# Optimization experiments

Hardware: AMD Instinct MI355X
Metric: run time of the kernel (lower is better)

## Reference

```python
import jax, jax.numpy as jnp
import numpy as np
import math

D_MODEL = 1024
NUM_HEADS = 16
MAX_LEN = 2048
D_HEAD = D_MODEL // NUM_HEADS
BATCH = 2
SEQ = 2048


def setup_inputs() -> dict:
    root = jax.random.key(0)
    ks = jax.random.split(root, 10)
    s = 1.0 / math.sqrt(D_MODEL)
    return {
        "query": jax.random.normal(ks[0], (BATCH, SEQ, D_MODEL), jnp.float32),
        "key": jax.random.normal(ks[1], (BATCH, SEQ, D_MODEL), jnp.float32),
        "value": jax.random.normal(ks[2], (BATCH, SEQ, D_MODEL), jnp.float32),
        "Wq": jax.random.normal(ks[3], (D_MODEL, D_MODEL), jnp.float32) * s,
        "bq": jax.random.normal(ks[4], (D_MODEL,), jnp.float32) * s,
        "Wk": jax.random.normal(ks[5], (D_MODEL, D_MODEL), jnp.float32) * s,
        "bk": jax.random.normal(ks[6], (D_MODEL,), jnp.float32) * s,
        "Wv": jax.random.normal(ks[7], (D_MODEL, D_MODEL), jnp.float32) * s,
        "bv": jax.random.normal(ks[8], (D_MODEL,), jnp.float32) * s,
        "Er": jax.random.normal(ks[9], (MAX_LEN, D_HEAD), jnp.float32),
    }


def _skew(QEr):
    # QEr: [B, H, S, S] -> pad one zero column on the left, reshape, drop first row
    B, H, R, C = QEr.shape
    padded = jnp.pad(QEr, ((0, 0), (0, 0), (0, 0), (1, 0)))  # [B,H,R,C+1]
    reshaped = padded.reshape(B, H, C + 1, R)
    return reshaped[:, :, 1:, :]  # [B,H,R,C] == Srel


def reference(query, key, value, Wq, bq, Wk, bk, Wv, bv, Er):
    B, S, D = query.shape
    H, dh = NUM_HEADS, D_HEAD
    # nn.Linear: x @ W.T + b
    q = (jnp.einsum("bsd,ed->bse", query, Wq) + bq).reshape(B, S, H, dh).transpose(0, 2, 1, 3)  # [B,H,S,dh]
    k = (jnp.einsum("bsd,ed->bse", key, Wk) + bk).reshape(B, S, H, dh).transpose(0, 2, 1, 3)
    v = (jnp.einsum("bsd,ed->bse", value, Wv) + bv).reshape(B, S, H, dh).transpose(0, 2, 1, 3)
    start = MAX_LEN - S
    Er_s = Er[start:, :]  # [S, dh]
    QEr = jnp.einsum("bhsd,ld->bhsl", q, Er_s)  # [B,H,S,S]
    Srel = _skew(QEr)
    QK = jnp.einsum("bhsd,bhtd->bhst", q, k)
    attn = (QK + Srel) / math.sqrt(dh)
    causal = jnp.tril(jnp.ones((S, S), dtype=bool))
    attn = jnp.where(causal[None, None], attn, -jnp.inf)
    attn = jax.nn.softmax(attn, axis=-1)
    out = jnp.einsum("bhst,bhtd->bhsd", attn, v)  # [B,H,S,dh]
    out = out.transpose(0, 2, 1, 3).reshape(B, S, D)
    return out  # dropout is identity in eval mode
```

## Files before the change

kernel.cpp:

```cpp
#include <hip/hip_runtime.h>
#include <hip/hip_bf16.h>

typedef __attribute__((ext_vector_type(8))) short bf16x8;
typedef __attribute__((ext_vector_type(4))) float f32x4;

#define DEVI __device__ __forceinline__

constexpr int SEQ_   = 2048;
constexpr int HEADS  = 16;
constexpr int DHEAD  = 64;
constexpr int DMODEL = 1024;

DEVI unsigned short f2bf(float x) {
  __hip_bfloat16 h = __float2bfloat16(x);
  return __builtin_bit_cast(unsigned short, h);
}

DEVI f32x4 MFMA(bf16x8 a, bf16x8 b, f32x4 c) {
  return __builtin_amdgcn_mfma_f32_16x16x32_bf16(a, b, c, 0, 0, 0);
}

__global__ void conv3_kernel(const float* s0, const float* s1, const float* s2,
                             unsigned short* d0, unsigned short* d1, unsigned short* d2,
                             int n) {
  const float* s = (blockIdx.y == 0) ? s0 : (blockIdx.y == 1) ? s1 : s2;
  unsigned short* d = (blockIdx.y == 0) ? d0 : (blockIdx.y == 1) ? d1 : d2;
  int i = (blockIdx.x * 256 + threadIdx.x) * 8;
  if (i >= n) return;
  const float4* p = (const float4*)(s + i);
  float4 v0 = p[0], v1 = p[1];
  union { unsigned short u[8]; bf16x8 v; } t;
  t.u[0] = f2bf(v0.x); t.u[1] = f2bf(v0.y); t.u[2] = f2bf(v0.z); t.u[3] = f2bf(v0.w);
  t.u[4] = f2bf(v1.x); t.u[5] = f2bf(v1.y); t.u[6] = f2bf(v1.z); t.u[7] = f2bf(v1.w);
  *(bf16x8*)(d + i) = t.v;
}

__global__ __launch_bounds__(256) void proj3_kernel(
    const unsigned short* __restrict__ X0, const unsigned short* __restrict__ X1,
    const unsigned short* __restrict__ X2,
    const unsigned short* __restrict__ W0, const unsigned short* __restrict__ W1,
    const unsigned short* __restrict__ W2,
    const float* __restrict__ bi0, const float* __restrict__ bi1,
    const float* __restrict__ bi2,
    unsigned short* __restrict__ o0, unsigned short* __restrict__ o1,
    unsigned short* __restrict__ o2) {
  const int z = blockIdx.z;
  const unsigned short* X = (z == 0) ? X0 : (z == 1) ? X1 : X2;
  const unsigned short* W = (z == 0) ? W0 : (z == 1) ? W1 : W2;
  const float* bias        = (z == 0) ? bi0 : (z == 1) ? bi1 : bi2;
  unsigned short* out      = (z == 0) ? o0 : (z == 1) ? o1 : o2;

  __shared__ unsigned short Abuf[2][128 * 32];
  __shared__ unsigned short Bbuf[2][128 * 32];
  const int tid  = threadIdx.x;
  const int lane = tid & 63, wv = tid >> 6;
  const int q = lane >> 4, r = lane & 15;
  const int wrow = wv >> 1, wcol = wv & 1;
  const int rowA0 = blockIdx.x * 128, colB0 = blockIdx.y * 128;

  const char* Ag = (const char*)(X + (size_t)rowA0 * DMODEL);
  const char* Bg = (const char*)(W + (size_t)colB0 * DMODEL);

  f32x4 acc[4][4] = {};

  auto stage = [&](int ks, int buf) {
    const int koff = ks * 64;
#pragma unroll
    for (int i = 0; i < 2; ++i) {
      const int b   = (i * 256 + tid) * 16;
      const int row = b >> 6, col = b & 63;
      __builtin_amdgcn_global_load_lds(
          (const __attribute__((address_space(1))) void*)(Ag + (size_t)row * (DMODEL * 2) + koff + col),
          (__attribute__((address_space(3))) void*)((char*)&Abuf[buf][0] + i * 4096 + wv * 1024),
          16, 0, 0);
      __builtin_amdgcn_global_load_lds(
          (const __attribute__((address_space(1))) void*)(Bg + (size_t)row * (DMODEL * 2) + koff + col),
          (__attribute__((address_space(3))) void*)((char*)&Bbuf[buf][0] + i * 4096 + wv * 1024),
          16, 0, 0);
    }
  };

  stage(0, 0);
  for (int ks = 0; ks < 32; ++ks) {
    __syncthreads();
    if (ks + 1 < 32) stage(ks + 1, (ks + 1) & 1);
    const unsigned short* A  = &Abuf[ks & 1][0];
    const unsigned short* Bt = &Bbuf[ks & 1][0];
    bf16x8 af[4], bfr[4];
#pragma unroll
    for (int t = 0; t < 4; ++t) {
      af[t]  = *(const bf16x8*)(A  + (wrow * 64 + t * 16 + r) * 32 + q * 8);
      bfr[t] = *(const bf16x8*)(Bt + (wcol * 64 + t * 16 + r) * 32 + q * 8);
    }
#pragma unroll
    for (int m = 0; m < 4; ++m)
#pragma unroll
      for (int n = 0; n < 4; ++n)
        acc[m][n] = MFMA(af[m], bfr[n], acc[m][n]);
  }

#pragma unroll
  for (int m = 0; m < 4; ++m) {
#pragma unroll
    for (int n = 0; n < 4; ++n) {
      const int e  = colB0 + wcol * 64 + n * 16 + r;
      const float bv = bias[e];
      const int h = e >> 6, dd = e & 63;
      const int nrow0 = rowA0 + wrow * 64 + m * 16 + q * 4;
      const int bb = nrow0 >> 11, ss0 = nrow0 & 2047;
      const size_t bh = (size_t)(bb * HEADS + h);
      if (z == 0) {
#pragma unroll
        for (int j = 0; j < 4; ++j)
          out[(bh * SEQ_ + (ss0 + j)) * DHEAD + dd] = f2bf(acc[m][n][j] + bv);
      } else if (z == 1) {
        const int kc = dd >> 5, d32 = dd & 31;
#pragma unroll
        for (int j = 0; j < 4; ++j) {
          const int s = ss0 + j;
          out[(((bh * 64 + (s >> 5)) * 2 + kc) * 32 + (s & 31)) * 32 + d32] =
              f2bf(acc[m][n][j] + bv);
        }
      } else {
        const int stile = ss0 >> 5, st = ss0 & 31;
        union { unsigned short u[4]; uint2 v; } pk;
#pragma unroll
        for (int j = 0; j < 4; ++j) pk.u[j] = f2bf(acc[m][n][j] + bv);
        *(uint2*)&out[((bh * 64 + stile) * 64 + dd) * 32 + st] = pk.v;
      }
    }
  }
}

__global__ __launch_bounds__(128, 2) void attn_kernel(const unsigned short* __restrict__ qb,
                                                      const unsigned short* __restrict__ kt,
                                                      const unsigned short* __restrict__ vt,
                                                      const unsigned short* __restrict__ Er,
                                                      float* __restrict__ out) {
  __shared__ unsigned short k_lds[2][2048];
  __shared__ unsigned short v_lds[2][2048];
  __shared__ unsigned short p_lds[2][16][40];

  const int tid  = threadIdx.x;
  const int lane = tid & 63, wv = tid >> 6;
  const int q = lane >> 4, r = lane & 15;

  const int lid = blockIdx.x;
  const int xcd = lid & 7, idx = lid >> 3;
  const int bh  = (xcd << 2) | (idx & 3);
  const int pairidx = idx >> 2;
  const int bb = bh >> 4, hh = bh & 15;

  const unsigned short* qbh = qb + (size_t)bh * SEQ_ * DHEAD;
  const char* ktb = (const char*)(kt + (size_t)bh * 64 * 2048);
  const char* vtb = (const char*)(vt + (size_t)bh * 64 * 2048);

  const f32x4 zero4 = {0.f, 0.f, 0.f, 0.f};

  auto stage = [&](int tile, int buf) {
#pragma unroll
    for (int c = 0; c < 2; ++c) {
      __builtin_amdgcn_global_load_lds(
          (const __attribute__((address_space(1))) void*)(ktb + (size_t)tile * 4096 + (c * 128 + tid) * 16),
          (__attribute__((address_space(3))) void*)((char*)&k_lds[buf][0] + c * 2048 + wv * 1024),
          16, 0, 0);
      __builtin_amdgcn_global_load_lds(
          (const __attribute__((address_space(1))) void*)(vtb + (size_t)tile * 4096 + (c * 128 + tid) * 16),
          (__attribute__((address_space(3))) void*)((char*)&v_lds[buf][0] + c * 2048 + wv * 1024),
          16, 0, 0);
    }
  };

#pragma unroll 1
  for (int si = 0; si < 2; ++si) {
    const int t = si ? pairidx : 63 - pairidx;
    const int nIter = t + 1;
    const int s0 = t * 32 + wv * 16;

    __syncthreads();
    stage(0, 0);

    bf16x8 qf0 = *(const bf16x8*)(qbh + (size_t)(s0 + r) * DHEAD + q * 8);
    bf16x8 qf1 = *(const bf16x8*)(qbh + (size_t)(s0 + r) * DHEAD + 32 + q * 8);

    f32x4 oacc[4] = {};
    float lpart[4] = {0.f, 0.f, 0.f, 0.f};
    f32x4 qer0;
    {
      const int l0 = 2032 - s0 + r;
      bf16x8 e00 = *(const bf16x8*)(Er + (size_t)l0 * DHEAD + q * 8);
      bf16x8 e01 = *(const bf16x8*)(Er + (size_t)l0 * DHEAD + 32 + q * 8);
      qer0 = MFMA(qf1, e01, MFMA(qf0, e00, zero4));
    }

#pragma unroll 1
    for (int it = 0; it < nIter; ++it) {
      const int cur = it & 1;
      const int t0 = it * 32;
      const int lbase = 2032 + t0 - s0;

      __syncthreads();

      int l1 = lbase + 16 + r; l1 = l1 < 2047 ? l1 : 2047;
      int l2 = lbase + 32 + r; l2 = l2 < 2047 ? l2 : 2047;
      bf16x8 e10 = *(const bf16x8*)(Er + (size_t)l1 * DHEAD + q * 8);
      bf16x8 e11 = *(const bf16x8*)(Er + (size_t)l1 * DHEAD + 32 + q * 8);
      bf16x8 e20 = *(const bf16x8*)(Er + (size_t)l2 * DHEAD + q * 8);
      bf16x8 e21 = *(const bf16x8*)(Er + (size_t)l2 * DHEAD + 32 + q * 8);

      if (it + 1 < nIter) stage(it + 1, 1 - cur);

      const unsigned short* KL = &k_lds[cur][0];
      const unsigned short* VL = &v_lds[cur][0];
      bf16x8 kf00 = *(const bf16x8*)(KL + r * 32 + q * 8);
      bf16x8 kf01 = *(const bf16x8*)(KL + 1024 + r * 32 + q * 8);
      bf16x8 kf10 = *(const bf16x8*)(KL + (16 + r) * 32 + q * 8);
      bf16x8 kf11 = *(const bf16x8*)(KL + 1024 + (16 + r) * 32 + q * 8);

      __builtin_amdgcn_s_setprio(1);
      f32x4 s40  = MFMA(qf1, kf01, MFMA(qf0, kf00, zero4));
      f32x4 s41  = MFMA(qf1, kf11, MFMA(qf0, kf10, zero4));
      f32x4 qer1 = MFMA(qf1, e11, MFMA(qf0, e10, zero4));
      f32x4 qer2 = MFMA(qf1, e21, MFMA(qf0, e20, zero4));
      __builtin_amdgcn_s_setprio(0);

#pragma unroll
      for (int j = 0; j < 4; ++j) {
        const int sl = q * 4 + j;
        const int idxw = r + 15 - sl;
        const int srcl = (q << 4) | (idxw & 15);
        const float g0 = __shfl(qer0[j], srcl);
        const float g1 = __shfl(qer1[j], srcl);
        const float g2 = __shfl(qer2[j], srcl);
        const bool lo = (idxw < 16);
        float sv0 = (s40[j] + (lo ? g0 : g1)) * 0.125f;
        float sv1 = (s41[j] + (lo ? g1 : g2)) * 0.125f;
        if (t0 + r      > s0 + sl) sv0 = -1e30f;
        if (t0 + 16 + r > s0 + sl) sv1 = -1e30f;
        const float p0 = __expf(sv0);
        const float p1 = __expf(sv1);
        lpart[j] += p0 + p1;
        p_lds[wv][sl][r]      = f2bf(p0);
        p_lds[wv][sl][16 + r] = f2bf(p1);
      }

      bf16x8 pf = *(const bf16x8*)(&p_lds[wv][r][0] + q * 8);
      bf16x8 vf0 = *(const bf16x8*)(VL + (r) * 32 + q * 8);
      bf16x8 vf1 = *(const bf16x8*)(VL + (16 + r) * 32 + q * 8);
      bf16x8 vf2 = *(const bf16x8*)(VL + (32 + r) * 32 + q * 8);
      bf16x8 vf3 = *(const bf16x8*)(VL + (48 + r) * 32 + q * 8);
      __builtin_amdgcn_s_setprio(1);
      oacc[0] = MFMA(pf, vf0, oacc[0]);
      oacc[1] = MFMA(pf, vf1, oacc[1]);
      oacc[2] = MFMA(pf, vf2, oacc[2]);
      oacc[3] = MFMA(pf, vf3, oacc[3]);
      __builtin_amdgcn_s_setprio(0);
      qer0 = qer2;
    }

#pragma unroll
    for (int j = 0; j < 4; ++j) {
      float ls = lpart[j];
#pragma unroll
      for (int d = 1; d < 16; d <<= 1) ls += __shfl_xor(ls, d);
      const float inv = 1.0f / ls;
      const int ss = s0 + q * 4 + j;
#pragma unroll
      for (int dc = 0; dc < 4; ++dc) {
        const int dd = dc * 16 + r;
        out[((size_t)(bb * SEQ_ + ss)) * DMODEL + hh * DHEAD + dd] = oacc[dc][j] * inv;
      }
    }
  }
}

extern "C" void kernel_launch(void* const* d_in, const int* in_sizes, int n_in,
                              void* d_out, int out_size, void* d_ws, size_t ws_size,
                              hipStream_t stream) {
  const float* query = (const float*)d_in[0];
  const float* key   = (const float*)d_in[1];
  const float* value = (const float*)d_in[2];
  const float* Wq    = (const float*)d_in[3];
  const float* bq    = (const float*)d_in[4];
  const float* Wk    = (const float*)d_in[5];
  const float* bk    = (const float*)d_in[6];
  const float* Wv    = (const float*)d_in[7];
  const float* bv    = (const float*)d_in[8];
  const float* Er    = (const float*)d_in[9];

  char* ws = (char*)d_ws;
  unsigned short* qb   = (unsigned short*)(ws + (0u  << 20));
  unsigned short* ktil = (unsigned short*)(ws + (8u  << 20));
  unsigned short* vtil = (unsigned short*)(ws + (16u << 20));
  unsigned short* Xq   = (unsigned short*)(ws + (32u << 20));
  unsigned short* Xk   = (unsigned short*)(ws + (40u << 20));
  unsigned short* Xv   = (unsigned short*)(ws + (48u << 20));
  unsigned short* Wqb  = (unsigned short*)(ws + (56u << 20));
  unsigned short* Wkb  = (unsigned short*)(ws + (58u << 20));
  unsigned short* Wvb  = (unsigned short*)(ws + (60u << 20));
  unsigned short* Erb  = (unsigned short*)(ws + (62u << 20));

  conv3_kernel<<<dim3(2048, 3), 256, 0, stream>>>(query, key, value, Xq, Xk, Xv,
                                                  2 * SEQ_ * DMODEL);
  conv3_kernel<<<dim3(512, 3), 256, 0, stream>>>(Wq, Wk, Wv, Wqb, Wkb, Wvb,
                                                 DMODEL * DMODEL);
  conv3_kernel<<<dim3(64, 1), 256, 0, stream>>>(Er, Er, Er, Erb, Erb, Erb,
                                                SEQ_ * DHEAD);

  proj3_kernel<<<dim3(32, 8, 3), 256, 0, stream>>>(Xq, Xk, Xv, Wqb, Wkb, Wvb,
                                                   bq, bk, bv, qb, ktil, vtil);

  attn_kernel<<<dim3(1024), 128, 0, stream>>>(qb, ktil, vtil, Erb, (float*)d_out);
}
```

Baseline: 146.0 us.

## Split long causal strips across blocks with partial-sum reduce and fragment-ordered K/V tiles

Each block previously processed a long and a short causal strip, 65 key tiles in total. The long strip is now split into two halves handled by separate blocks. This doubles the grid and gives each block roughly 33 tiles. The halves write unnormalized partial outputs and row sums to workspace, and a new reduce kernel adds them and normalizes. The projection kernel now writes K and V tiles in an MFMA-fragment order so each lane reads LDS contiguously, and the attention kernel's launch bounds are raised to 4 blocks per SIMD. The cost is an extra kernel launch plus about 16 MB of partial-result traffic.

```diff
diff --git a/kernel.cpp b/kernel.cpp
--- a/kernel.cpp
+++ b/kernel.cpp
@@ -114,29 +114,36 @@
         for (int j = 0; j < 4; ++j)
           out[(bh * SEQ_ + (ss0 + j)) * DHEAD + dd] = f2bf(acc[m][n][j] + bv);
       } else if (z == 1) {
-        const int kc = dd >> 5, d32 = dd & 31;
 #pragma unroll
         for (int j = 0; j < 4; ++j) {
           const int s = ss0 + j;
-          out[(((bh * 64 + (s >> 5)) * 2 + kc) * 32 + (s & 31)) * 32 + d32] =
-              f2bf(acc[m][n][j] + bv);
+          const size_t off = (bh * 64 + (size_t)(s >> 5)) * 2048
+                           + (size_t)(((dd >> 5) * 2 + ((s >> 4) & 1)) * 512)
+                           + (size_t)(((((dd & 31) >> 3) << 4) + (s & 15)) * 8)
+                           + (dd & 7);
+          out[off] = f2bf(acc[m][n][j] + bv);
         }
       } else {
-        const int stile = ss0 >> 5, st = ss0 & 31;
         union { unsigned short u[4]; uint2 v; } pk;
 #pragma unroll
         for (int j = 0; j < 4; ++j) pk.u[j] = f2bf(acc[m][n][j] + bv);
-        *(uint2*)&out[((bh * 64 + stile) * 64 + dd) * 32 + st] = pk.v;
+        const size_t off = (bh * 64 + (size_t)(ss0 >> 5)) * 2048
+                         + (size_t)((dd >> 4) * 512)
+                         + (size_t)(((((ss0 & 31) >> 3) << 4) + (dd & 15)) * 8)
+                         + (ss0 & 7);
+        *(uint2*)&out[off] = pk.v;
       }
     }
   }
 }
 
-__global__ __launch_bounds__(128, 2) void attn_kernel(const unsigned short* __restrict__ qb,
+__global__ __launch_bounds__(128, 4) void attn_kernel(const unsigned short* __restrict__ qb,
                                                       const unsigned short* __restrict__ kt,
                                                       const unsigned short* __restrict__ vt,
                                                       const unsigned short* __restrict__ Er,
-                                                      float* __restrict__ out) {
+                                                      float* __restrict__ out,
+                                                      float* __restrict__ pO,
+                                                      float* __restrict__ pL) {
   __shared__ unsigned short k_lds[2][2048];
   __shared__ unsigned short v_lds[2][2048];
   __shared__ unsigned short p_lds[2][16][40];
@@ -148,7 +155,10 @@
   const int lid = blockIdx.x;
   const int xcd = lid & 7, idx = lid >> 3;
   const int bh  = (xcd << 2) | (idx & 3);
-  const int pairidx = idx >> 2;
+  const int rest = idx >> 2;
+  const int p = rest >> 1, ab = rest & 1;
+  const int Lt = 63 - p;
+  const int sid = (bh << 5) | p;
   const int bb = bh >> 4, hh = bh & 15;
 
   const unsigned short* qbh = qb + (size_t)bh * SEQ_ * DHEAD;
@@ -157,28 +167,24 @@
 
   const f32x4 zero4 = {0.f, 0.f, 0.f, 0.f};
 
-  auto stage = [&](int tile, int buf) {
+  auto stage = [&](int ktile, int buf) {
 #pragma unroll
     for (int c = 0; c < 2; ++c) {
       __builtin_amdgcn_global_load_lds(
-          (const __attribute__((address_space(1))) void*)(ktb + (size_t)tile * 4096 + (c * 128 + tid) * 16),
+          (const __attribute__((address_space(1))) void*)(ktb + (size_t)ktile * 4096 + (c * 128 + tid) * 16),
           (__attribute__((address_space(3))) void*)((char*)&k_lds[buf][0] + c * 2048 + wv * 1024),
           16, 0, 0);
       __builtin_amdgcn_global_load_lds(
-          (const __attribute__((address_space(1))) void*)(vtb + (size_t)tile * 4096 + (c * 128 + tid) * 16),
+          (const __attribute__((address_space(1))) void*)(vtb + (size_t)ktile * 4096 + (c * 128 + tid) * 16),
           (__attribute__((address_space(3))) void*)((char*)&v_lds[buf][0] + c * 2048 + wv * 1024),
           16, 0, 0);
     }
   };
 
-#pragma unroll 1
-  for (int si = 0; si < 2; ++si) {
-    const int t = si ? pairidx : 63 - pairidx;
-    const int nIter = t + 1;
-    const int s0 = t * 32 + wv * 16;
-
+  auto run_strip = [&](int tile, int it0, int itN, float* po, float* pl) {
+    const int s0 = tile * 32 + wv * 16;
     __syncthreads();
-    stage(0, 0);
+    stage(it0, 0);
 
     bf16x8 qf0 = *(const bf16x8*)(qbh + (size_t)(s0 + r) * DHEAD + q * 8);
     bf16x8 qf1 = *(const bf16x8*)(qbh + (size_t)(s0 + r) * DHEAD + 32 + q * 8);
@@ -187,15 +193,15 @@
     float lpart[4] = {0.f, 0.f, 0.f, 0.f};
     f32x4 qer0;
     {
-      const int l0 = 2032 - s0 + r;
+      const int l0 = 2032 + it0 * 32 - s0 + r;
       bf16x8 e00 = *(const bf16x8*)(Er + (size_t)l0 * DHEAD + q * 8);
       bf16x8 e01 = *(const bf16x8*)(Er + (size_t)l0 * DHEAD + 32 + q * 8);
       qer0 = MFMA(qf1, e01, MFMA(qf0, e00, zero4));
     }
 
 #pragma unroll 1
-    for (int it = 0; it < nIter; ++it) {
-      const int cur = it & 1;
+    for (int it = it0; it < itN; ++it) {
+      const int cur = (it - it0) & 1;
       const int t0 = it * 32;
       const int lbase = 2032 + t0 - s0;
 
@@ -208,14 +214,14 @@
       bf16x8 e20 = *(const bf16x8*)(Er + (size_t)l2 * DHEAD + q * 8);
       bf16x8 e21 = *(const bf16x8*)(Er + (size_t)l2 * DHEAD + 32 + q * 8);
 
-      if (it + 1 < nIter) stage(it + 1, 1 - cur);
+      if (it + 1 < itN) stage(it + 1, 1 - cur);
 
       const unsigned short* KL = &k_lds[cur][0];
       const unsigned short* VL = &v_lds[cur][0];
-      bf16x8 kf00 = *(const bf16x8*)(KL + r * 32 + q * 8);
-      bf16x8 kf01 = *(const bf16x8*)(KL + 1024 + r * 32 + q * 8);
-      bf16x8 kf10 = *(const bf16x8*)(KL + (16 + r) * 32 + q * 8);
-      bf16x8 kf11 = *(const bf16x8*)(KL + 1024 + (16 + r) * 32 + q * 8);
+      bf16x8 kf00 = *(const bf16x8*)(KL + lane * 8);
+      bf16x8 kf10 = *(const bf16x8*)(KL + 512 + lane * 8);
+      bf16x8 kf01 = *(const bf16x8*)(KL + 1024 + lane * 8);
+      bf16x8 kf11 = *(const bf16x8*)(KL + 1536 + lane * 8);
 
       __builtin_amdgcn_s_setprio(1);
       f32x4 s40  = MFMA(qf1, kf01, MFMA(qf0, kf00, zero4));
@@ -244,11 +250,11 @@
         p_lds[wv][sl][16 + r] = f2bf(p1);
       }
 
-      bf16x8 pf = *(const bf16x8*)(&p_lds[wv][r][0] + q * 8);
-      bf16x8 vf0 = *(const bf16x8*)(VL + (r) * 32 + q * 8);
-      bf16x8 vf1 = *(const bf16x8*)(VL + (16 + r) * 32 + q * 8);
-      bf16x8 vf2 = *(const bf16x8*)(VL + (32 + r) * 32 + q * 8);
-      bf16x8 vf3 = *(const bf16x8*)(VL + (48 + r) * 32 + q * 8);
+      bf16x8 pf  = *(const bf16x8*)(&p_lds[wv][r][0] + q * 8);
+      bf16x8 vf0 = *(const bf16x8*)(VL + lane * 8);
+      bf16x8 vf1 = *(const bf16x8*)(VL + 512 + lane * 8);
+      bf16x8 vf2 = *(const bf16x8*)(VL + 1024 + lane * 8);
+      bf16x8 vf3 = *(const bf16x8*)(VL + 1536 + lane * 8);
       __builtin_amdgcn_s_setprio(1);
       oacc[0] = MFMA(pf, vf0, oacc[0]);
       oacc[1] = MFMA(pf, vf1, oacc[1]);
@@ -263,15 +269,59 @@
       float ls = lpart[j];
 #pragma unroll
       for (int d = 1; d < 16; d <<= 1) ls += __shfl_xor(ls, d);
-      const float inv = 1.0f / ls;
-      const int ss = s0 + q * 4 + j;
-#pragma unroll
-      for (int dc = 0; dc < 4; ++dc) {
-        const int dd = dc * 16 + r;
-        out[((size_t)(bb * SEQ_ + ss)) * DMODEL + hh * DHEAD + dd] = oacc[dc][j] * inv;
+      const int row = wv * 16 + q * 4 + j;
+      if (po) {
+#pragma unroll
+        for (int dc = 0; dc < 4; ++dc)
+          po[(size_t)row * 64 + dc * 16 + r] = oacc[dc][j];
+        if (r == 0) pl[row] = ls;
+      } else {
+        const float inv = 1.0f / ls;
+        const int ss = tile * 32 + row;
+#pragma unroll
+        for (int dc = 0; dc < 4; ++dc) {
+          const int dd = dc * 16 + r;
+          out[((size_t)(bb * SEQ_ + ss)) * DMODEL + hh * DHEAD + dd] = oacc[dc][j] * inv;
+        }
       }
     }
+  };
+
+  if (ab == 0) {
+    run_strip(Lt, 0, 32, pO + (size_t)(sid * 2) * 2048, pL + (size_t)(sid * 2) * 32);
+  } else {
+    run_strip(Lt, 32, 64 - p, pO + (size_t)(sid * 2 + 1) * 2048, pL + (size_t)(sid * 2 + 1) * 32);
+    run_strip(p, 0, p + 1, nullptr, nullptr);
   }
+}
+
+__global__ __launch_bounds__(256) void reduce_kernel(const float* __restrict__ pO,
+                                                     const float* __restrict__ pL,
+                                                     float* __restrict__ out) {
+  const int sid = blockIdx.x;
+  const int bh = sid >> 5, p = sid & 31;
+  const int bb = bh >> 4, hh = bh & 15;
+  const int srow = (63 - p) * 32;
+  const int tid = threadIdx.x;
+  const int row = tid >> 3, dseg = (tid & 7) * 8;
+
+  const float* a = pO + (size_t)(sid * 2) * 2048 + row * 64 + dseg;
+  const float* b = a + 2048;
+  const float la = pL[(size_t)(sid * 2) * 32 + row];
+  const float lb = pL[(size_t)(sid * 2 + 1) * 32 + row];
+  const float inv = 1.0f / (la + lb);
+
+  float4 x0 = ((const float4*)a)[0], x1 = ((const float4*)a)[1];
+  float4 y0 = ((const float4*)b)[0], y1 = ((const float4*)b)[1];
+  float4 o0, o1;
+  o0.x = (x0.x + y0.x) * inv; o0.y = (x0.y + y0.y) * inv;
+  o0.z = (x0.z + y0.z) * inv; o0.w = (x0.w + y0.w) * inv;
+  o1.x = (x1.x + y1.x) * inv; o1.y = (x1.y + y1.y) * inv;
+  o1.z = (x1.z + y1.z) * inv; o1.w = (x1.w + y1.w) * inv;
+
+  float* dst = out + ((size_t)(bb * SEQ_) + srow + row) * DMODEL + hh * DHEAD + dseg;
+  ((float4*)dst)[0] = o0;
+  ((float4*)dst)[1] = o1;
 }
 
 extern "C" void kernel_launch(void* const* d_in, const int* in_sizes, int n_in,
@@ -292,6 +342,8 @@
   unsigned short* qb   = (unsigned short*)(ws + (0u  << 20));
   unsigned short* ktil = (unsigned short*)(ws + (8u  << 20));
   unsigned short* vtil = (unsigned short*)(ws + (16u << 20));
+  float*          pO   = (float*)(ws + (24u << 20));
+  float*          pL   = (float*)(ws + (40u << 20));
   unsigned short* Xq   = (unsigned short*)(ws + (32u << 20));
   unsigned short* Xk   = (unsigned short*)(ws + (40u << 20));
   unsigned short* Xv   = (unsigned short*)(ws + (48u << 20));
@@ -310,5 +362,8 @@
   proj3_kernel<<<dim3(32, 8, 3), 256, 0, stream>>>(Xq, Xk, Xv, Wqb, Wkb, Wvb,
                                                    bq, bk, bv, qb, ktil, vtil);
 
-  attn_kernel<<<dim3(1024), 128, 0, stream>>>(qb, ktil, vtil, Erb, (float*)d_out);
-}
+  attn_kernel<<<dim3(2048), 128, 0, stream>>>(qb, ktil, vtil, Erb,
+                                              (float*)d_out, pO, pL);
+
+  reduce_kernel<<<dim3(1024), 256, 0, stream>>>(pO, pL, (float*)d_out);
+}
```

Result: slower. 155.3 us (+6.4%).
